# Kernel tuning notes

Hardware: AMD Instinct MI355X
Metric: run time of the kernel (lower is better)

The kernel has to match this reference:

```python
import jax, jax.numpy as jnp
import numpy as np

N_NODES = 50000
N_EDGES = 600000
D = 128
EDGE_DIM = 1
N_LAYERS = 2
NEG_SLOPE = 0.2


def setup_inputs() -> dict:
    key = jax.random.key(0)
    ks = jax.random.split(key, 8)
    x = jax.random.normal(ks[0], (N_NODES, D), dtype=jnp.float32)
    edge_index = jax.random.randint(ks[1], (2, N_EDGES), 0, N_NODES, dtype=jnp.int64)
    edge_attr = jax.random.normal(ks[2], (N_EDGES, EDGE_DIM), dtype=jnp.float32)
    s = 1.0 / np.sqrt(D)
    Wl = jax.random.normal(ks[3], (N_LAYERS, D, D), dtype=jnp.float32) * s   # lin_l weights
    Wr = jax.random.normal(ks[4], (N_LAYERS, D, D), dtype=jnp.float32) * s   # lin_r weights
    We = jax.random.normal(ks[5], (N_LAYERS, EDGE_DIM, D), dtype=jnp.float32) * s  # lin_edge
    att = jax.random.normal(ks[6], (N_LAYERS, D), dtype=jnp.float32) * s     # attention vector (heads=1)
    bias = jnp.zeros((N_LAYERS, D), dtype=jnp.float32)
    return {"x": x, "edge_index": edge_index, "edge_attr": edge_attr,
            "Wl": Wl, "Wr": Wr, "We": We, "att": att, "bias": bias}


def _gatv2_layer(x, src, dst, edge_attr, Wl, Wr, We, att, bias):
    # GATv2Conv, heads=1, add_self_loops=False, share_weights=False.
    xl = x @ Wl                                   # [N, D] (source transform)
    xr = x @ Wr                                   # [N, D] (target transform)
    m = xl[src] + xr[dst] + edge_attr @ We        # [E, D]
    m = jax.nn.leaky_relu(m, NEG_SLOPE)
    logits = m @ att                              # [E]
    # segment softmax over incoming edges of each dst node
    mx = jax.ops.segment_max(logits, dst, num_segments=N_NODES)  # [N]
    ex = jnp.exp(logits - mx[dst])                # [E]
    denom = jax.ops.segment_sum(ex, dst, num_segments=N_NODES)   # [N]
    alpha = ex / jnp.maximum(denom[dst], 1e-16)   # [E]
    out = jax.ops.segment_sum(alpha[:, None] * xl[src], dst, num_segments=N_NODES)
    return out + bias


def reference(x, edge_index, edge_attr, Wl, Wr, We, att, bias):
    src, dst = edge_index[0], edge_index[1]
    h = x
    for l in range(N_LAYERS):
        h = _gatv2_layer(h, src, dst, edge_attr, Wl[l], Wr[l], We[l], att[l], bias[l])
        h = jax.nn.relu(h)   # activation; norm=None, dropout=0 (eval) are identity
    return h
```

## Files before the change

kernel.cpp:

```cpp
#include <hip/hip_runtime.h>
#include <hip/hip_fp16.h>

#define N_NODES 50000
#define N_PAD   50048
#define N_EDGES 600000
#define DD 128
#define NEG_SLOPE 0.2f
#define BSHIFT 7
#define NBUCKETS 391
#define MAXB 2048

typedef _Float16 h2 __attribute__((ext_vector_type(2)));
typedef _Float16 h8 __attribute__((ext_vector_type(8)));
typedef __attribute__((ext_vector_type(4))) float f32x4;
typedef unsigned long long u64;

__device__ inline h2 bch2(unsigned u) { return __builtin_bit_cast(h2, u); }
__device__ inline unsigned h2u(h2 h) { return __builtin_bit_cast(unsigned, h); }
__device__ inline ushort f2h_bits(float x) {
    return __builtin_bit_cast(ushort, (_Float16)x);
}

#if __has_builtin(__builtin_amdgcn_fdot2)
#define DOT2(a, b, c) __builtin_amdgcn_fdot2((a), (b), (c), false)
#else
#define DOT2(a, b, c) ((c) + (float)(a)[0] * (float)(b)[0] + (float)(a)[1] * (float)(b)[1])
#endif

__global__ void detect_zero_kernel(const int* __restrict__ ei, int* __restrict__ flag,
                                   int* __restrict__ bcount) {
    int t = threadIdx.x;
    if (t < NBUCKETS) bcount[t] = 0;
    if (t == 0) {
        int is64 = 1;
        for (int i = 0; i < 64; ++i) {
            if (ei[2 * i + 1] != 0) { is64 = 0; break; }
        }
        *flag = is64;
    }
}

__global__ __launch_bounds__(512) void bin_edges(
    const int* __restrict__ ei, const int* __restrict__ flag,
    const float* __restrict__ ea, int* __restrict__ bcount,
    u64* __restrict__ tmp) {
    __shared__ int lhist[NBUCKETS];
    __shared__ int lbase[NBUCKETS];
    for (int i = threadIdx.x; i < NBUCKETS; i += 512) lhist[i] = 0;
    __syncthreads();
    const bool is64 = (*flag) != 0;
    int base = blockIdx.x * 4096;
    int myb[8], myrank[8];
    u64 mypack[8];
    #pragma unroll
    for (int i = 0; i < 8; ++i) {
        int e = base + i * 512 + threadIdx.x;
        if (e < N_EDGES) {
            int s, d;
            if (is64) {
                const long long* e64 = (const long long*)ei;
                s = (int)e64[e];
                d = (int)e64[N_EDGES + e];
            } else {
                s = ei[e];
                d = ei[N_EDGES + e];
            }
            unsigned hb = (unsigned)f2h_bits(ea[e]);
            int b = d >> BSHIFT;
            myb[i] = b;
            mypack[i] = ((u64)(unsigned)(d & 127) << 32) | ((u64)hb << 16) | (unsigned)s;
            myrank[i] = atomicAdd(&lhist[b], 1);
        } else myb[i] = -1;
    }
    __syncthreads();
    for (int i = threadIdx.x; i < NBUCKETS; i += 512) {
        int c = lhist[i];
        lbase[i] = c ? atomicAdd(&bcount[i], c) : 0;
    }
    __syncthreads();
    #pragma unroll
    for (int i = 0; i < 8; ++i)
        if (myb[i] >= 0) {
            int rel = lbase[myb[i]] + myrank[i];
            if (rel < MAXB)
                tmp[(size_t)myb[i] * MAXB + rel] = mypack[i];
        }
}

__global__ void scan_buckets(const int* __restrict__ bcount, int* __restrict__ bucket_off,
                             int* __restrict__ row_start) {
    __shared__ int s[512];
    int i = threadIdx.x;
    int v = (i < NBUCKETS) ? min(bcount[i], MAXB) : 0;
    s[i] = v;
    __syncthreads();
    #pragma unroll
    for (int off = 1; off < 512; off <<= 1) {
        int t = (i >= off) ? s[i - off] : 0;
        __syncthreads();
        s[i] += t;
        __syncthreads();
    }
    if (i < NBUCKETS) bucket_off[i] = s[i] - v;
    if (i == NBUCKETS - 1) row_start[N_NODES] = s[i];
}

__global__ __launch_bounds__(256) void scatter_sort(
    const u64* __restrict__ tmp, const int* __restrict__ bcount,
    const int* __restrict__ bucket_off,
    unsigned* __restrict__ se_csr, int* __restrict__ row_start) {
    __shared__ int lcnt[128];
    __shared__ int lscan[128];
    __shared__ int lcur[128];
    int b = blockIdx.x;
    int tid = threadIdx.x;
    if (tid < 128) lcnt[tid] = 0;
    __syncthreads();
    int n_e = bcount[b]; if (n_e > MAXB) n_e = MAXB;
    const u64* tb = tmp + (size_t)b * MAXB;
    for (int e = tid; e < n_e; e += 256)
        atomicAdd(&lcnt[(int)(tb[e] >> 32)], 1);
    __syncthreads();
    if (tid < 128) lscan[tid] = lcnt[tid];
    __syncthreads();
    #pragma unroll
    for (int off = 1; off < 128; off <<= 1) {
        int t = 0;
        if (tid < 128 && tid >= off) t = lscan[tid - off];
        __syncthreads();
        if (tid < 128) lscan[tid] += t;
        __syncthreads();
    }
    int boff = bucket_off[b];
    int nb = b << BSHIFT;
    if (tid < 128) {
        int start = boff + lscan[tid] - lcnt[tid];
        lcur[tid] = start;
        if (nb + tid < N_NODES) row_start[nb + tid] = start;
    }
    __syncthreads();
    for (int e = tid; e < n_e; e += 256) {
        u64 w = tb[e];
        int pos = atomicAdd(&lcur[(int)(w >> 32)], 1);
        se_csr[pos] = (unsigned)w;
    }
}

__global__ void pack_W(const float* __restrict__ Wl, const float* __restrict__ Wr,
                       ushort* __restrict__ Wp) {
    int idx = blockIdx.x * 256 + threadIdx.x;
    if (idx >= 65536) return;
    int layer = idx >> 15;
    int which = (idx >> 14) & 1;
    int kk    = (idx >> 12) & 3;
    int c     = (idx >> 9) & 7;
    int lane  = (idx >> 3) & 63;
    int j     = idx & 7;
    int k   = kk * 32 + (lane >> 4) * 8 + j;
    int col = c * 16 + (lane & 15);
    const float* W = which ? Wr : Wl;
    Wp[idx] = f2h_bits(W[(size_t)layer * DD * DD + k * DD + col]);
}

template<bool AF32>
__global__ __launch_bounds__(256) void gemm_mfma(
    const ushort* __restrict__ h, const float* __restrict__ xf,
    const ushort* __restrict__ Wp,
    ushort* __restrict__ xl, ushort* __restrict__ xr) {
    __shared__ ushort wlds[32768];
    #pragma unroll
    for (int i = 0; i < 16; ++i) {
        int idx = i * 256 + threadIdx.x;
        ((uint4*)wlds)[idx] = ((const uint4*)Wp)[idx];
    }
    int wave = threadIdx.x >> 6, lane = threadIdx.x & 63;
    int arow = blockIdx.x * 64 + wave * 16 + (lane & 15);
    int kbase = (lane >> 4) * 8;
    f32x4 accl[8], accr[8];
    #pragma unroll
    for (int c = 0; c < 8; ++c) {
        accl[c] = (f32x4){0.f, 0.f, 0.f, 0.f};
        accr[c] = (f32x4){0.f, 0.f, 0.f, 0.f};
    }
    __syncthreads();
    #pragma unroll
    for (int kk = 0; kk < 4; ++kk) {
        h8 a;
        if (AF32) {
            if (arow < N_NODES) {
                const float* xp = xf + (size_t)arow * DD + kk * 32 + kbase;
                float4 u0 = *(const float4*)xp;
                float4 u1 = *(const float4*)(xp + 4);
                a[0] = (_Float16)u0.x; a[1] = (_Float16)u0.y;
                a[2] = (_Float16)u0.z; a[3] = (_Float16)u0.w;
                a[4] = (_Float16)u1.x; a[5] = (_Float16)u1.y;
                a[6] = (_Float16)u1.z; a[7] = (_Float16)u1.w;
            } else {
                #pragma unroll
                for (int i = 0; i < 8; ++i) a[i] = (_Float16)0.f;
            }
        } else {
            a = *(const h8*)&h[(size_t)arow * DD + kk * 32 + kbase];
        }
        #pragma unroll
        for (int c = 0; c < 8; ++c) {
            h8 bl = *(const h8*)&wlds[((kk * 8 + c) * 64 + lane) * 8];
            h8 br = *(const h8*)&wlds[16384 + ((kk * 8 + c) * 64 + lane) * 8];
            accl[c] = __builtin_amdgcn_mfma_f32_16x16x32_f16(a, bl, accl[c], 0, 0, 0);
            accr[c] = __builtin_amdgcn_mfma_f32_16x16x32_f16(a, br, accr[c], 0, 0, 0);
        }
    }
    ushort* tile = wlds;
    int drow = wave * 16 + ((lane >> 4) << 2);
    int dcol = lane & 15;
    #pragma unroll
    for (int half = 0; half < 2; ++half) {
        const f32x4* acc = half ? accr : accl;
        ushort* out = half ? xr : xl;
        __syncthreads();
        #pragma unroll
        for (int c = 0; c < 8; ++c)
            #pragma unroll
            for (int r = 0; r < 4; ++r)
                tile[(drow + r) * 136 + c * 16 + dcol] = f2h_bits(acc[c][r]);
        __syncthreads();
        #pragma unroll
        for (int it = 0; it < 8; ++it) {
            int i = it * 256 + threadIdx.x;
            int row = i >> 5, cc = (i & 31) * 4;
            int gr = blockIdx.x * 64 + row;
            if (gr < N_NODES)
                *(ushort4*)&out[(size_t)gr * DD + cc] = *(const ushort4*)&tile[row * 136 + cc];
        }
    }
}

template<bool OUT_F16>
__global__ __launch_bounds__(256) void fused_node_f16(
    const ushort* __restrict__ xl, const ushort* __restrict__ xr,
    const float* __restrict__ We, const float* __restrict__ att,
    const int* __restrict__ row_start, const unsigned* __restrict__ se_csr,
    const float* __restrict__ bias, void* __restrict__ outp) {
    int wave = threadIdx.x >> 6;
    int lane = threadIdx.x & 63;
    int n = blockIdx.x * 4 + wave;
    if (n >= N_NODES) return;
    int g  = lane >> 4;
    int cb = (lane & 15) * 8;

    uint4 xrv = *(const uint4*)&xr[(size_t)n * DD + cb];
    h2 xr2[4] = {bch2(xrv.x), bch2(xrv.y), bch2(xrv.z), bch2(xrv.w)};
    float4 wf0 = *(const float4*)&We[cb], wf1 = *(const float4*)&We[cb + 4];
    float4 af0 = *(const float4*)&att[cb], af1 = *(const float4*)&att[cb + 4];
    h2 We2[4] = {{(_Float16)wf0.x, (_Float16)wf0.y}, {(_Float16)wf0.z, (_Float16)wf0.w},
                 {(_Float16)wf1.x, (_Float16)wf1.y}, {(_Float16)wf1.z, (_Float16)wf1.w}};
    h2 at2[4] = {{(_Float16)af0.x, (_Float16)af0.y}, {(_Float16)af0.z, (_Float16)af0.w},
                 {(_Float16)af1.x, (_Float16)af1.y}, {(_Float16)af1.z, (_Float16)af1.w}};
    const h2 ns2 = {(_Float16)NEG_SLOPE, (_Float16)NEG_SLOPE};

    int beg = row_start[n], end = row_start[n + 1];
    h2 acc2[4];
    #pragma unroll
    for (int k = 0; k < 4; ++k) acc2[k] = (h2){(_Float16)0.f, (_Float16)0.f};
    float denom = 0.f;

    for (int j = beg; j < end; j += 16) {
        unsigned w[4]; bool vl[4]; uint4 xv[4];
        #pragma unroll
        for (int q = 0; q < 4; ++q) {
            int e = j + 4 * q + g;
            vl[q] = e < end;
            w[q] = se_csr[vl[q] ? e : (end - 1)];
        }
        #pragma unroll
        for (int q = 0; q < 4; ++q)
            xv[q] = *(const uint4*)&xl[(size_t)(w[q] & 0xffffu) * DD + cb];
        h2 xq[4][4];
        float part[4];
        #pragma unroll
        for (int q = 0; q < 4; ++q) {
            xq[q][0] = bch2(xv[q].x); xq[q][1] = bch2(xv[q].y);
            xq[q][2] = bch2(xv[q].z); xq[q][3] = bch2(xv[q].w);
            h2 a2 = bch2((w[q] >> 16) * 0x10001u);
            float pd = 0.f;
            #pragma unroll
            for (int k = 0; k < 4; ++k) {
                h2 m = __builtin_elementwise_fma(a2, We2[k], xq[q][k] + xr2[k]);
                m = __builtin_elementwise_max(m, m * ns2);
                pd = DOT2(m, at2[k], pd);
            }
            part[q] = pd;
        }
        #pragma unroll
        for (int o = 1; o < 16; o <<= 1) {
            #pragma unroll
            for (int q = 0; q < 4; ++q) part[q] += __shfl_xor(part[q], o, 64);
        }
        #pragma unroll
        for (int q = 0; q < 4; ++q) {
            float p = vl[q] ? __expf(part[q]) : 0.f;
            denom += p;
            _Float16 ph = (_Float16)p;
            h2 p2 = {ph, ph};
            #pragma unroll
            for (int k = 0; k < 4; ++k)
                acc2[k] = __builtin_elementwise_fma(p2, xq[q][k], acc2[k]);
        }
    }

    #pragma unroll
    for (int o = 16; o < 64; o <<= 1) {
        #pragma unroll
        for (int k = 0; k < 4; ++k) {
            int t = __shfl_xor(__builtin_bit_cast(int, acc2[k]), o, 64);
            acc2[k] += __builtin_bit_cast(h2, t);
        }
        denom += __shfl_xor(denom, o, 64);
    }

    if (g == 0) {
        float inv = 1.0f / fmaxf(denom, 1e-16f);
        float o_[8];
        #pragma unroll
        for (int k = 0; k < 4; ++k) {
            o_[2 * k]     = fmaxf(fmaf((float)acc2[k][0], inv, bias[cb + 2 * k]), 0.f);
            o_[2 * k + 1] = fmaxf(fmaf((float)acc2[k][1], inv, bias[cb + 2 * k + 1]), 0.f);
        }
        if (OUT_F16) {
            uint4 o4;
            o4.x = h2u((h2){(_Float16)o_[0], (_Float16)o_[1]});
            o4.y = h2u((h2){(_Float16)o_[2], (_Float16)o_[3]});
            o4.z = h2u((h2){(_Float16)o_[4], (_Float16)o_[5]});
            o4.w = h2u((h2){(_Float16)o_[6], (_Float16)o_[7]});
            *(uint4*)((ushort*)outp + (size_t)n * DD + cb) = o4;
        } else {
            float* op = (float*)outp + (size_t)n * DD + cb;
            *(float4*)op       = *(float4*)&o_[0];
            *(float4*)(op + 4) = *(float4*)&o_[4];
        }
    }
}

extern "C" void kernel_launch(void* const* d_in, const int* in_sizes, int n_in,
                              void* d_out, int out_size, void* d_ws, size_t ws_size,
                              hipStream_t stream) {
    const float* x    = (const float*)d_in[0];
    const int*   ei   = (const int*)d_in[1];
    const float* ea   = (const float*)d_in[2];
    const float* Wl   = (const float*)d_in[3];
    const float* Wr   = (const float*)d_in[4];
    const float* We   = (const float*)d_in[5];
    const float* att  = (const float*)d_in[6];
    const float* bias = (const float*)d_in[7];

    char* wsb = (char*)d_ws;
    size_t off = 0;
    auto alloc = [&](size_t bytes) { void* r = (void*)(wsb + off); off += (bytes + 15) & ~15ull; return r; };
    ushort* h_f16    = (ushort*)alloc((size_t)N_PAD * DD * 2);
    ushort* xl_f16   = (ushort*)alloc((size_t)N_NODES * DD * 2);
    ushort* xr_f16   = (ushort*)alloc((size_t)N_NODES * DD * 2);
    ushort* Wp       = (ushort*)alloc(65536 * 2);
    u64*    tmp      = (u64*)alloc((size_t)NBUCKETS * MAXB * 8);
    unsigned* se_csr = (unsigned*)alloc((size_t)N_EDGES * 4);
    int*    row_st   = (int*)alloc((N_NODES + 1) * 4);
    int*    bcount   = (int*)alloc(NBUCKETS * 4);
    int*    boff     = (int*)alloc(NBUCKETS * 4);
    int*    flag     = (int*)alloc(4);

    detect_zero_kernel<<<1, 512, 0, stream>>>(ei, flag, bcount);

    bin_edges<<<(N_EDGES + 4095) / 4096, 512, 0, stream>>>(ei, flag, ea, bcount, tmp);
    scan_buckets<<<1, 512, 0, stream>>>(bcount, boff, row_st);
    scatter_sort<<<NBUCKETS, 256, 0, stream>>>(tmp, bcount, boff, se_csr, row_st);

    pack_W<<<256, 256, 0, stream>>>(Wl, Wr, Wp);

    const int ggrid = N_PAD / 64;
    for (int l = 0; l < 2; ++l) {
        const ushort* Wp_l  = Wp + (size_t)l * 32768;
        const float* We_l   = We + (size_t)l * DD;
        const float* att_l  = att + (size_t)l * DD;
        const float* bias_l = bias + (size_t)l * DD;

        if (l == 0) {
            gemm_mfma<true><<<ggrid, 256, 0, stream>>>(nullptr, x, Wp_l, xl_f16, xr_f16);
            fused_node_f16<true><<<(N_NODES + 3) / 4, 256, 0, stream>>>(
                xl_f16, xr_f16, We_l, att_l, row_st, se_csr, bias_l, (void*)h_f16);
        } else {
            gemm_mfma<false><<<ggrid, 256, 0, stream>>>(h_f16, nullptr, Wp_l, xl_f16, xr_f16);
            fused_node_f16<false><<<(N_NODES + 3) / 4, 256, 0, stream>>>(
                xl_f16, xr_f16, We_l, att_l, row_st, se_csr, bias_l, d_out);
        }
    }
}
```

Before: 130.3 us.

## Merge setup kernels, fold bucket scan into scatter, split GEMM weight staging

Folds the zero-detect and weight-packing kernels into one launch and moves the bucket prefix scan into every scatter_sort block, which removes two kernel launches and their serialization gaps. The GEMM now stages only half the weights in shared memory at a time (32 KB instead of 64 KB) and loads its A rows before staging, with the aim of raising occupancy. It also adds a min-blocks hint of 8 to the node kernel. In exchange, each scatter block repeats the small scan, the GEMM gains extra barriers, and the occupancy hint may force register spills.

```diff
diff --git a/kernel.cpp b/kernel.cpp
--- a/kernel.cpp
+++ b/kernel.cpp
@@ -27,17 +27,32 @@
 #define DOT2(a, b, c) ((c) + (float)(a)[0] * (float)(b)[0] + (float)(a)[1] * (float)(b)[1])
 #endif
 
-__global__ void detect_zero_kernel(const int* __restrict__ ei, int* __restrict__ flag,
-                                   int* __restrict__ bcount) {
-    int t = threadIdx.x;
-    if (t < NBUCKETS) bcount[t] = 0;
-    if (t == 0) {
-        int is64 = 1;
-        for (int i = 0; i < 64; ++i) {
-            if (ei[2 * i + 1] != 0) { is64 = 0; break; }
-        }
-        *flag = is64;
-    }
+__global__ void pack_detect(const float* __restrict__ Wl, const float* __restrict__ Wr,
+                            ushort* __restrict__ Wp,
+                            const int* __restrict__ ei, int* __restrict__ flag,
+                            int* __restrict__ bcount) {
+    if (blockIdx.x == 256) {
+        for (int t = threadIdx.x; t < NBUCKETS; t += 256) bcount[t] = 0;
+        if (threadIdx.x == 0) {
+            int is64 = 1;
+            for (int i = 0; i < 64; ++i) {
+                if (ei[2 * i + 1] != 0) { is64 = 0; break; }
+            }
+            *flag = is64;
+        }
+        return;
+    }
+    int idx = blockIdx.x * 256 + threadIdx.x;
+    int layer = idx >> 15;
+    int which = (idx >> 14) & 1;
+    int kk    = (idx >> 12) & 3;
+    int c     = (idx >> 9) & 7;
+    int lane  = (idx >> 3) & 63;
+    int j     = idx & 7;
+    int k   = kk * 32 + (lane >> 4) * 8 + j;
+    int col = c * 16 + (lane & 15);
+    const float* W = which ? Wr : Wl;
+    Wp[idx] = f2h_bits(W[(size_t)layer * DD * DD + k * DD + col]);
 }
 
 __global__ __launch_bounds__(512) void bin_edges(
@@ -87,33 +102,36 @@
         }
 }
 
-__global__ void scan_buckets(const int* __restrict__ bcount, int* __restrict__ bucket_off,
-                             int* __restrict__ row_start) {
-    __shared__ int s[512];
-    int i = threadIdx.x;
-    int v = (i < NBUCKETS) ? min(bcount[i], MAXB) : 0;
-    s[i] = v;
-    __syncthreads();
-    #pragma unroll
-    for (int off = 1; off < 512; off <<= 1) {
-        int t = (i >= off) ? s[i - off] : 0;
-        __syncthreads();
-        s[i] += t;
-        __syncthreads();
-    }
-    if (i < NBUCKETS) bucket_off[i] = s[i] - v;
-    if (i == NBUCKETS - 1) row_start[N_NODES] = s[i];
-}
-
 __global__ __launch_bounds__(256) void scatter_sort(
     const u64* __restrict__ tmp, const int* __restrict__ bcount,
-    const int* __restrict__ bucket_off,
     unsigned* __restrict__ se_csr, int* __restrict__ row_start) {
+    __shared__ int bscan[512];
     __shared__ int lcnt[128];
     __shared__ int lscan[128];
     __shared__ int lcur[128];
+    int tid = threadIdx.x;
+    {
+        int v = 0;
+        if (tid < NBUCKETS) { v = bcount[tid]; if (v > MAXB) v = MAXB; }
+        bscan[tid] = v;
+        int v2 = 0;
+        if (tid + 256 < NBUCKETS) { v2 = bcount[tid + 256]; if (v2 > MAXB) v2 = MAXB; }
+        bscan[tid + 256] = v2;
+    }
+    __syncthreads();
+    #pragma unroll
+    for (int off = 1; off < 512; off <<= 1) {
+        int t0 = (tid >= off) ? bscan[tid - off] : 0;
+        int t1 = (tid + 256 >= off) ? bscan[tid + 256 - off] : 0;
+        __syncthreads();
+        bscan[tid] += t0;
+        bscan[tid + 256] += t1;
+        __syncthreads();
+    }
     int b = blockIdx.x;
-    int tid = threadIdx.x;
+    int boff = (b == 0) ? 0 : bscan[b - 1];
+    if (b == 0 && tid == 0) row_start[N_NODES] = bscan[NBUCKETS - 1];
+
     if (tid < 128) lcnt[tid] = 0;
     __syncthreads();
     int n_e = bcount[b]; if (n_e > MAXB) n_e = MAXB;
@@ -131,7 +149,6 @@
         if (tid < 128) lscan[tid] += t;
         __syncthreads();
     }
-    int boff = bucket_off[b];
     int nb = b << BSHIFT;
     if (tid < 128) {
         int start = boff + lscan[tid] - lcnt[tid];
@@ -146,70 +163,68 @@
     }
 }
 
-__global__ void pack_W(const float* __restrict__ Wl, const float* __restrict__ Wr,
-                       ushort* __restrict__ Wp) {
-    int idx = blockIdx.x * 256 + threadIdx.x;
-    if (idx >= 65536) return;
-    int layer = idx >> 15;
-    int which = (idx >> 14) & 1;
-    int kk    = (idx >> 12) & 3;
-    int c     = (idx >> 9) & 7;
-    int lane  = (idx >> 3) & 63;
-    int j     = idx & 7;
-    int k   = kk * 32 + (lane >> 4) * 8 + j;
-    int col = c * 16 + (lane & 15);
-    const float* W = which ? Wr : Wl;
-    Wp[idx] = f2h_bits(W[(size_t)layer * DD * DD + k * DD + col]);
-}
-
 template<bool AF32>
 __global__ __launch_bounds__(256) void gemm_mfma(
     const ushort* __restrict__ h, const float* __restrict__ xf,
     const ushort* __restrict__ Wp,
     ushort* __restrict__ xl, ushort* __restrict__ xr) {
-    __shared__ ushort wlds[32768];
-    #pragma unroll
-    for (int i = 0; i < 16; ++i) {
-        int idx = i * 256 + threadIdx.x;
-        ((uint4*)wlds)[idx] = ((const uint4*)Wp)[idx];
-    }
+    __shared__ ushort wlds[16384];
     int wave = threadIdx.x >> 6, lane = threadIdx.x & 63;
     int arow = blockIdx.x * 64 + wave * 16 + (lane & 15);
     int kbase = (lane >> 4) * 8;
-    f32x4 accl[8], accr[8];
-    #pragma unroll
-    for (int c = 0; c < 8; ++c) {
-        accl[c] = (f32x4){0.f, 0.f, 0.f, 0.f};
-        accr[c] = (f32x4){0.f, 0.f, 0.f, 0.f};
-    }
-    __syncthreads();
+
+    h8 a[4];
     #pragma unroll
     for (int kk = 0; kk < 4; ++kk) {
-        h8 a;
         if (AF32) {
             if (arow < N_NODES) {
                 const float* xp = xf + (size_t)arow * DD + kk * 32 + kbase;
                 float4 u0 = *(const float4*)xp;
                 float4 u1 = *(const float4*)(xp + 4);
-                a[0] = (_Float16)u0.x; a[1] = (_Float16)u0.y;
-                a[2] = (_Float16)u0.z; a[3] = (_Float16)u0.w;
-                a[4] = (_Float16)u1.x; a[5] = (_Float16)u1.y;
-                a[6] = (_Float16)u1.z; a[7] = (_Float16)u1.w;
+                a[kk][0] = (_Float16)u0.x; a[kk][1] = (_Float16)u0.y;
+                a[kk][2] = (_Float16)u0.z; a[kk][3] = (_Float16)u0.w;
+                a[kk][4] = (_Float16)u1.x; a[kk][5] = (_Float16)u1.y;
+                a[kk][6] = (_Float16)u1.z; a[kk][7] = (_Float16)u1.w;
             } else {
                 #pragma unroll
-                for (int i = 0; i < 8; ++i) a[i] = (_Float16)0.f;
+                for (int i = 0; i < 8; ++i) a[kk][i] = (_Float16)0.f;
             }
         } else {
-            a = *(const h8*)&h[(size_t)arow * DD + kk * 32 + kbase];
-        }
+            a[kk] = *(const h8*)&h[(size_t)arow * DD + kk * 32 + kbase];
+        }
+    }
+
+    #pragma unroll
+    for (int i = 0; i < 8; ++i)
+        ((uint4*)wlds)[i * 256 + threadIdx.x] = ((const uint4*)Wp)[i * 256 + threadIdx.x];
+    f32x4 accl[8], accr[8];
+    #pragma unroll
+    for (int c = 0; c < 8; ++c) {
+        accl[c] = (f32x4){0.f, 0.f, 0.f, 0.f};
+        accr[c] = (f32x4){0.f, 0.f, 0.f, 0.f};
+    }
+    __syncthreads();
+    #pragma unroll
+    for (int kk = 0; kk < 4; ++kk)
         #pragma unroll
         for (int c = 0; c < 8; ++c) {
             h8 bl = *(const h8*)&wlds[((kk * 8 + c) * 64 + lane) * 8];
-            h8 br = *(const h8*)&wlds[16384 + ((kk * 8 + c) * 64 + lane) * 8];
-            accl[c] = __builtin_amdgcn_mfma_f32_16x16x32_f16(a, bl, accl[c], 0, 0, 0);
-            accr[c] = __builtin_amdgcn_mfma_f32_16x16x32_f16(a, br, accr[c], 0, 0, 0);
-        }
-    }
+            accl[c] = __builtin_amdgcn_mfma_f32_16x16x32_f16(a[kk], bl, accl[c], 0, 0, 0);
+        }
+    __syncthreads();
+
+    #pragma unroll
+    for (int i = 0; i < 8; ++i)
+        ((uint4*)wlds)[i * 256 + threadIdx.x] = ((const uint4*)(Wp + 16384))[i * 256 + threadIdx.x];
+    __syncthreads();
+    #pragma unroll
+    for (int kk = 0; kk < 4; ++kk)
+        #pragma unroll
+        for (int c = 0; c < 8; ++c) {
+            h8 br = *(const h8*)&wlds[((kk * 8 + c) * 64 + lane) * 8];
+            accr[c] = __builtin_amdgcn_mfma_f32_16x16x32_f16(a[kk], br, accr[c], 0, 0, 0);
+        }
+
     ushort* tile = wlds;
     int drow = wave * 16 + ((lane >> 4) << 2);
     int dcol = lane & 15;
@@ -236,7 +251,7 @@
 }
 
 template<bool OUT_F16>
-__global__ __launch_bounds__(256) void fused_node_f16(
+__global__ __launch_bounds__(256, 8) void fused_node_f16(
     const ushort* __restrict__ xl, const ushort* __restrict__ xr,
     const float* __restrict__ We, const float* __restrict__ att,
     const int* __restrict__ row_start, const unsigned* __restrict__ se_csr,
@@ -364,16 +379,12 @@
     unsigned* se_csr = (unsigned*)alloc((size_t)N_EDGES * 4);
     int*    row_st   = (int*)alloc((N_NODES + 1) * 4);
     int*    bcount   = (int*)alloc(NBUCKETS * 4);
-    int*    boff     = (int*)alloc(NBUCKETS * 4);
     int*    flag     = (int*)alloc(4);
 
-    detect_zero_kernel<<<1, 512, 0, stream>>>(ei, flag, bcount);
+    pack_detect<<<257, 256, 0, stream>>>(Wl, Wr, Wp, ei, flag, bcount);
 
     bin_edges<<<(N_EDGES + 4095) / 4096, 512, 0, stream>>>(ei, flag, ea, bcount, tmp);
-    scan_buckets<<<1, 512, 0, stream>>>(bcount, boff, row_st);
-    scatter_sort<<<NBUCKETS, 256, 0, stream>>>(tmp, bcount, boff, se_csr, row_st);
-
-    pack_W<<<256, 256, 0, stream>>>(Wl, Wr, Wp);
+    scatter_sort<<<NBUCKETS, 256, 0, stream>>>(tmp, bcount, se_csr, row_st);
 
     const int ggrid = N_PAD / 64;
     for (int l = 0; l < 2; ++l) {
```

Result: slower. 135.3 us (+3.8%).
